# Kernel tuning notes

Hardware: AMD Instinct MI355X
Metric: run time of the kernel (lower is better)

Reference implementation:

```python
import jax, jax.numpy as jnp
import numpy as np

B, T, C = 4, 2048, 1024
H = 16
DH = C // H


def setup_inputs() -> dict:
    key = jax.random.key(0)
    k1, k2, k3 = jax.random.split(key, 3)
    x = jax.random.normal(k1, (B, T, C), dtype=jnp.float32)
    w_qkv = jax.random.normal(k2, (3 * C, C), dtype=jnp.float32) * (1.0 / np.sqrt(C))
    w_out = jax.random.normal(k3, (C, C), dtype=jnp.float32) * (1.0 / np.sqrt(C))
    attn_mask = jnp.ones((B, T), dtype=jnp.int32)
    return {"x": x, "attn_mask": attn_mask, "w_qkv": w_qkv, "w_out": w_out}


def reference(x, attn_mask, w_qkv, w_out):
    b, t, c = x.shape
    h, dh = H, DH
    qkv = jnp.einsum('btc,fc->btf', x, w_qkv)  # [B,T,3C]
    q, k, v = jnp.split(qkv, 3, axis=-1)
    # [B,H,T,Dh]
    q = q.reshape(b, t, h, dh).transpose(0, 2, 1, 3)
    k = k.reshape(b, t, h, dh).transpose(0, 2, 1, 3)
    v = v.reshape(b, t, h, dh).transpose(0, 2, 1, 3)
    scale = jnp.sqrt(jnp.float32(dh))
    scores = jnp.einsum('bhqd,bhkd->bhqk', q, k) / scale  # [B,H,T,T]
    causal = jnp.tril(jnp.ones((t, t), dtype=bool))
    mask = causal[None, None, :, :] & (attn_mask[:, None, None, :] != 0)
    scores = jnp.where(mask, scores, -jnp.inf)
    p = jax.nn.softmax(scores, axis=-1)
    p = jnp.where(jnp.isnan(p), 0.0, p)  # nan_to_num for fully-masked rows
    out = jnp.einsum('bhqk,bhkd->bhqd', p, v)
    out = out.transpose(0, 2, 1, 3).reshape(b, t, c)
    return jnp.einsum('btc,fc->btf', out, w_out)
```

## Files before the change

kernel.cpp:

```cpp
#include <hip/hip_runtime.h>
#include <cstdint>
#include <cmath>


#define Bb 4
#define Tt 2048
#define Cc 1024
#define Hh 16
#define DHd 64
#define Mm (Bb*Tt)

typedef __attribute__((ext_vector_type(8))) short bf16x8;
typedef __attribute__((ext_vector_type(4))) short s16x4;
typedef __attribute__((ext_vector_type(4))) float f32x4;
typedef __attribute__((ext_vector_type(2))) unsigned int u32x2;

__device__ __forceinline__ short f2bf(float f) {
  uint32_t u = __builtin_bit_cast(uint32_t, f);
  u = (u + 0x7fffu + ((u >> 16) & 1u)) >> 16;
  return (short)(uint16_t)u;
}

__device__ __forceinline__ uint32_t cvtpk(float lo, float hi) {
  uint32_t r;
  asm("v_cvt_pk_bf16_f32 %0, %1, %2" : "=v"(r) : "v"(lo), "v"(hi));
  return r;
}

__device__ __forceinline__ f32x4 mfma16(s16x4 a, s16x4 b, f32x4 c) {
#if __has_builtin(__builtin_amdgcn_mfma_f32_16x16x16_bf16)
  return __builtin_amdgcn_mfma_f32_16x16x16_bf16(a, b, c, 0, 0, 0);
#elif __has_builtin(__builtin_amdgcn_mfma_f32_16x16x16bf16_1k)
  return __builtin_amdgcn_mfma_f32_16x16x16bf16_1k(a, b, c, 0, 0, 0);
#else
  f32x4 d;
  asm("v_mfma_f32_16x16x16_bf16 %0, %1, %2, %3" : "=v"(d) : "v"(a), "v"(b), "v"(c));
  return d;
#endif
}

__global__ void cvt_bf16(const float* __restrict__ in, short* __restrict__ out, int n4) {
  int i = blockIdx.x * blockDim.x + threadIdx.x;
  if (i >= n4) return;
  f32x4 v = reinterpret_cast<const f32x4*>(in)[i];
  s16x4 o;
  o.x = f2bf(v.x); o.y = f2bf(v.y); o.z = f2bf(v.z); o.w = f2bf(v.w);
  reinterpret_cast<s16x4*>(out)[i] = o;
}

#define BK 32

template<int MODE>
__global__ __launch_bounds__(256) void gemm_bt(
    const short* __restrict__ A, const short* __restrict__ Bt, int K, int N,
    float* __restrict__ Cout,
    short* __restrict__ qb, short* __restrict__ kb, short* __restrict__ vtb)
{
  __shared__ __align__(16) short As[128*BK];
  __shared__ __align__(16) short Bs[128*BK];
  const int tid = threadIdx.x;
  const int lane = tid & 63, wid = tid >> 6;
  const int wr = wid >> 1, wc = wid & 1;
  const int bm = blockIdx.y, bn = blockIdx.x;
  const int r16 = lane & 15, g = lane >> 4;

  f32x4 acc[4][4];
#pragma unroll
  for (int i = 0; i < 4; ++i)
#pragma unroll
    for (int j = 0; j < 4; ++j) acc[i][j] = (f32x4)0.0f;

  const int srow = lane >> 2;
  const int scol = (lane & 3) * 8;
  const int ch0 = wid * 2;

  const int nk = K / BK;
  for (int kt = 0; kt < nk; ++kt) {
    const int k0 = kt * BK;
#pragma unroll
    for (int c = 0; c < 2; ++c) {
      const int chunk = ch0 + c;
      const int row = chunk * 16 + srow;
      const short* ga = A  + (size_t)(bm*128 + row)*K + k0 + scol;
      const short* gb = Bt + (size_t)(bn*128 + row)*K + k0 + scol;
      __builtin_amdgcn_global_load_lds((const __attribute__((address_space(1))) void*)ga,
                                       (__attribute__((address_space(3))) void*)(&As[chunk*512]), 16, 0, 0);
      __builtin_amdgcn_global_load_lds((const __attribute__((address_space(1))) void*)gb,
                                       (__attribute__((address_space(3))) void*)(&Bs[chunk*512]), 16, 0, 0);
    }
    __syncthreads();

    bf16x8 af[4], bfv[4];
#pragma unroll
    for (int mi = 0; mi < 4; ++mi)
      af[mi] = *reinterpret_cast<const bf16x8*>(&As[(wr*64 + mi*16 + r16)*BK + g*8]);
#pragma unroll
    for (int ni = 0; ni < 4; ++ni)
      bfv[ni] = *reinterpret_cast<const bf16x8*>(&Bs[(wc*64 + ni*16 + r16)*BK + g*8]);
#pragma unroll
    for (int mi = 0; mi < 4; ++mi)
#pragma unroll
      for (int ni = 0; ni < 4; ++ni)
        acc[mi][ni] = __builtin_amdgcn_mfma_f32_16x16x32_bf16(af[mi], bfv[ni], acc[mi][ni], 0, 0, 0);
    __syncthreads();
  }

#pragma unroll
  for (int mi = 0; mi < 4; ++mi) {
    const int row0 = bm*128 + wr*64 + mi*16 + g*4;
#pragma unroll
    for (int ni = 0; ni < 4; ++ni) {
      const int col_g = bn*128 + wc*64 + ni*16 + r16;
      if (MODE == 1) {
#pragma unroll
        for (int r = 0; r < 4; ++r)
          Cout[(size_t)(row0 + r) * N + col_g] = acc[mi][ni][r];
      } else {
        const int which = col_g >> 10;
        const int hd = col_g & 1023;
        const int h = hd >> 6, d = hd & 63;
        const int b = row0 >> 11, t0 = row0 & 2047;
        const int bh = b*Hh + h;
        if (which == 0) {
#pragma unroll
          for (int r = 0; r < 4; ++r)
            qb[(((size_t)bh*Tt + t0 + r) << 6) + d] = f2bf(acc[mi][ni][r] * 0.18033688f);
        } else if (which == 1) {
#pragma unroll
          for (int r = 0; r < 4; ++r)
            kb[(((size_t)bh*Tt + t0 + r) << 6) + d] = f2bf(acc[mi][ni][r]);
        } else {
          u32x2 w;
          w.x = cvtpk(acc[mi][ni][0], acc[mi][ni][1]);
          w.y = cvtpk(acc[mi][ni][2], acc[mi][ni][3]);
          *reinterpret_cast<u32x2*>(vtb + ((size_t)bh*DHd + d)*Tt + t0) = w;
        }
      }
    }
  }
}

__global__ __launch_bounds__(256) void attn_fwd(
    const short* __restrict__ qbf, const short* __restrict__ kbf,
    const short* __restrict__ vtb, const int* __restrict__ am,
    short* __restrict__ ob)
{
  __shared__ __align__(16) short Ks[2][64*64];
  __shared__ __align__(16) short Vts[2][64*64];
  const int tid = threadIdx.x;
  const int lane = tid & 63, wid = tid >> 6;
  const int r16 = lane & 15, g = lane >> 4;

  const int lin = blockIdx.x;
  const int xcd = lin & 7;
  const int idx = lin >> 3;
  const int bh  = xcd * 8 + (idx & 7);
  const int qi_raw = idx >> 3;
  const int grp = qi_raw >> 2, rem = qi_raw & 3;
  const int qi = (grp == 0) ? 15 - rem : (grp == 1) ? rem : (grp == 2) ? 11 - rem : 4 + rem;
  const int b = bh >> 4, h = bh & 15;
  const int q0 = qi * 128;
  const int wq0 = q0 + wid * 32;

  bf16x8 qf[2][2];
#pragma unroll
  for (int m = 0; m < 2; ++m) {
    const short* qbase = qbf + ((size_t)bh*Tt + wq0 + m*16 + r16)*DHd;
    qf[m][0] = *reinterpret_cast<const bf16x8*>(qbase + g*8);
    qf[m][1] = *reinterpret_cast<const bf16x8*>(qbase + 32 + g*8);
  }

  f32x4 o[2][4];
  float mrow[2], lrow[2];
#pragma unroll
  for (int m = 0; m < 2; ++m) {
    mrow[m] = -INFINITY; lrow[m] = 0.f;
#pragma unroll
    for (int i = 0; i < 4; ++i) o[m][i] = (f32x4)0.0f;
  }

  const int nkv = 2*qi + 2;
  const int srow = tid >> 3, scc = tid & 7;
  bf16x8 kr[2], vr[2];
#pragma unroll
  for (int c = 0; c < 2; ++c) {
    const int row = srow + c*32;
    kr[c] = *reinterpret_cast<const bf16x8*>(kbf + ((size_t)bh*Tt + row)*DHd + scc*8);
    vr[c] = *reinterpret_cast<const bf16x8*>(vtb + ((size_t)bh*DHd + row)*Tt + scc*8);
  }
#pragma unroll
  for (int c = 0; c < 2; ++c) {
    const int row = srow + c*32;
    const int off = (row*128 + scc*16) ^ ((row & 7) << 4);
    *reinterpret_cast<bf16x8*>((char*)Ks[0] + off) = kr[c];
    *reinterpret_cast<bf16x8*>((char*)Vts[0] + off) = vr[c];
  }
  __syncthreads();

  for (int kv = 0; kv < nkv; ++kv) {
    const int cur = kv & 1;
    const int kv0 = kv * 64;
    const unsigned long long mb = __ballot(am[b*Tt + kv0 + lane] != 0);
    if (kv + 1 < nkv) {
#pragma unroll
      for (int c = 0; c < 2; ++c) {
        const int row = srow + c*32;
        kr[c] = *reinterpret_cast<const bf16x8*>(kbf + ((size_t)bh*Tt + kv0 + 64 + row)*DHd + scc*8);
        vr[c] = *reinterpret_cast<const bf16x8*>(vtb + ((size_t)bh*DHd + row)*Tt + kv0 + 64 + scc*8);
      }
    }

    if (kv0 <= wq0 + 31) {
      const char* kbp = (const char*)Ks[cur];
      const char* vbp = (const char*)Vts[cur];
      const int swzr = (r16 & 7) << 4;

      f32x4 st[2][4];
      __builtin_amdgcn_s_setprio(1);
#pragma unroll
      for (int kt = 0; kt < 4; ++kt) {
        const int rb = (kt*16 + r16)*128;
        const bf16x8 ka0 = *reinterpret_cast<const bf16x8*>(kbp + ((rb + g*16) ^ swzr));
        const bf16x8 ka1 = *reinterpret_cast<const bf16x8*>(kbp + ((rb + 64 + g*16) ^ swzr));
#pragma unroll
        for (int m = 0; m < 2; ++m) {
          f32x4 t = (f32x4)0.0f;
          t = __builtin_amdgcn_mfma_f32_16x16x32_bf16(ka0, qf[m][0], t, 0, 0, 0);
          t = __builtin_amdgcn_mfma_f32_16x16x32_bf16(ka1, qf[m][1], t, 0, 0, 0);
          st[m][kt] = t;
        }
      }
      __builtin_amdgcn_s_setprio(0);

      const bool notall = (mb != ~0ull);
      const bool diag = (kv0 + 63 > wq0);
      if (diag || notall) {
#pragma unroll
        for (int m = 0; m < 2; ++m) {
          const int qrow = wq0 + m*16 + r16;
#pragma unroll
          for (int kt = 0; kt < 4; ++kt)
#pragma unroll
            for (int r = 0; r < 4; ++r) {
              const int kl = kt*16 + g*4 + r;
              bool ok = !diag || (kv0 + kl <= qrow);
              if (notall) ok = ok && ((mb >> kl) & 1ull);
              if (!ok) st[m][kt][r] = -3.0e38f;
            }
        }
      }

      float mx[2], rs[2];
#pragma unroll
      for (int m = 0; m < 2; ++m) {
        f32x4 t0, t1;
#pragma unroll
        for (int i = 0; i < 4; ++i) { t0[i] = fmaxf(st[m][0][i], st[m][1][i]); t1[i] = fmaxf(st[m][2][i], st[m][3][i]); }
#pragma unroll
        for (int i = 0; i < 4; ++i) t0[i] = fmaxf(t0[i], t1[i]);
        mx[m] = fmaxf(fmaxf(t0[0], t0[1]), fmaxf(t0[2], t0[3]));
      }
      {
        float a0 = __shfl_xor(mx[0], 16), a1 = __shfl_xor(mx[1], 16);
        mx[0] = fmaxf(mx[0], a0); mx[1] = fmaxf(mx[1], a1);
        a0 = __shfl_xor(mx[0], 32); a1 = __shfl_xor(mx[1], 32);
        mx[0] = fmaxf(mx[0], a0); mx[1] = fmaxf(mx[1], a1);
      }
      const bool need = __any((mx[0] > mrow[0] + 8.f) || (mx[1] > mrow[1] + 8.f));
      if (need) {
#pragma unroll
        for (int m = 0; m < 2; ++m) {
          const float mnew = fmaxf(mrow[m], mx[m]);
          const float alpha = __builtin_amdgcn_exp2f(mrow[m] - mnew);
          mrow[m] = mnew;
          lrow[m] *= alpha;
#pragma unroll
          for (int dt = 0; dt < 4; ++dt) o[m][dt] *= alpha;
        }
      }

      s16x4 pb[2][4];
#pragma unroll
      for (int m = 0; m < 2; ++m) {
#pragma unroll
        for (int kt = 0; kt < 4; ++kt)
#pragma unroll
          for (int r = 0; r < 4; ++r)
            st[m][kt][r] = __builtin_amdgcn_exp2f(st[m][kt][r] - mrow[m]);
#pragma unroll
        for (int kt = 0; kt < 4; ++kt) {
          u32x2 w;
          w.x = cvtpk(st[m][kt][0], st[m][kt][1]);
          w.y = cvtpk(st[m][kt][2], st[m][kt][3]);
          pb[m][kt] = __builtin_bit_cast(s16x4, w);
        }
        f32x4 s4;
#pragma unroll
        for (int i = 0; i < 4; ++i) s4[i] = st[m][0][i] + st[m][1][i] + st[m][2][i] + st[m][3][i];
        rs[m] = (s4[0] + s4[1]) + (s4[2] + s4[3]);
      }
      {
        float a0 = __shfl_xor(rs[0], 16), a1 = __shfl_xor(rs[1], 16);
        rs[0] += a0; rs[1] += a1;
        a0 = __shfl_xor(rs[0], 32); a1 = __shfl_xor(rs[1], 32);
        rs[0] += a0; rs[1] += a1;
      }
      lrow[0] += rs[0]; lrow[1] += rs[1];

      __builtin_amdgcn_s_setprio(1);
#pragma unroll
      for (int dt = 0; dt < 4; ++dt) {
        const int row = dt*16 + r16;
        const int rb = row*128;
        const int r7 = row & 7;
#pragma unroll
        for (int kt = 0; kt < 4; ++kt) {
          const s16x4 va = *reinterpret_cast<const s16x4*>(
              vbp + rb + ((((kt<<1) + (g>>1)) ^ r7) << 4) + (g & 1)*8);
          o[0][dt] = mfma16(va, pb[0][kt], o[0][dt]);
          o[1][dt] = mfma16(va, pb[1][kt], o[1][dt]);
        }
      }
      __builtin_amdgcn_s_setprio(0);
    }

    if (kv + 1 < nkv) {
#pragma unroll
      for (int c = 0; c < 2; ++c) {
        const int row = srow + c*32;
        const int off = (row*128 + scc*16) ^ ((row & 7) << 4);
        *reinterpret_cast<bf16x8*>((char*)Ks[cur^1] + off) = kr[c];
        *reinterpret_cast<bf16x8*>((char*)Vts[cur^1] + off) = vr[c];
      }
    }
    __syncthreads();
  }

#pragma unroll
  for (int m = 0; m < 2; ++m) {
    const float inv = (mrow[m] > -1e37f) ? 1.0f / lrow[m] : 0.f;
    short* obase = ob + ((size_t)(b*Tt + wq0 + m*16 + r16))*Cc + h*DHd;
#pragma unroll
    for (int dt = 0; dt < 4; ++dt) {
      u32x2 w;
      w.x = cvtpk(o[m][dt][0]*inv, o[m][dt][1]*inv);
      w.y = cvtpk(o[m][dt][2]*inv, o[m][dt][3]*inv);
      *reinterpret_cast<u32x2*>(obase + dt*16 + g*4) = w;
    }
  }
}

extern "C" void kernel_launch(void* const* d_in, const int* in_sizes, int n_in,
                              void* d_out, int out_size, void* d_ws, size_t ws_size,
                              hipStream_t stream) {
  const float* x    = (const float*)d_in[0];
  const int*   am   = (const int*)d_in[1];
  const float* wqkv = (const float*)d_in[2];
  const float* wout = (const float*)d_in[3];
  float* out = (float*)d_out;

  const size_t mc = (size_t)Mm * Cc;
  short* ws    = (short*)d_ws;
  short* xb    = ws;
  short* wqkvb = xb + mc;
  short* woutb = wqkvb + (size_t)3*Cc*Cc;
  short* qbuf  = woutb + (size_t)Cc*Cc;
  short* kbuf  = qbuf + mc;
  short* vtbuf = kbuf + mc;
  short* attnb = xb;

  cvt_bf16<<<(int)((mc/4 + 255)/256), 256, 0, stream>>>(x, xb, (int)(mc/4));
  cvt_bf16<<<(3*Cc*Cc/4 + 255)/256, 256, 0, stream>>>(wqkv, wqkvb, 3*Cc*Cc/4);
  cvt_bf16<<<(Cc*Cc/4 + 255)/256, 256, 0, stream>>>(wout, woutb, Cc*Cc/4);

  gemm_bt<0><<<dim3(3*Cc/128, Mm/128), 256, 0, stream>>>(
      xb, wqkvb, Cc, 3*Cc, nullptr, qbuf, kbuf, vtbuf);

  attn_fwd<<<dim3(Bb*Hh*Tt/128), 256, 0, stream>>>(qbuf, kbuf, vtbuf, am, attnb);

  gemm_bt<1><<<dim3(Cc/128, Mm/128), 256, 0, stream>>>(
      attnb, woutb, Cc, Cc, out, nullptr, nullptr, nullptr);
}
```

Baseline: 218.3 us.

## Stage K/V tiles via direct global-to-LDS loads and prefetch mask

Replaces the register-staged K/V tile loads and later LDS stores in the attention kernel with global_load_lds direct-to-LDS transfers into the next buffer. The XOR swizzle moves from the LDS write address to the global read address. The attention-mask element for the next tile is also prefetched one iteration early. This is meant to cut VGPR pressure and the explicit LDS store instructions, at the cost of depending on the barrier to cover completion of the async LDS writes.

```diff
diff --git a/kernel.cpp b/kernel.cpp
--- a/kernel.cpp
+++ b/kernel.cpp
@@ -162,6 +162,29 @@
   const int q0 = qi * 128;
   const int wq0 = q0 + wid * 32;
 
+  const size_t kbase = (size_t)bh * Tt * DHd;
+  const size_t vbase = (size_t)bh * DHd * Tt;
+
+  const int srow0 = tid >> 3;
+  const int p8    = tid & 7;
+  const int ubase = tid & 448;
+
+#define ASTAGE(SLOT, T0) do {                                                  \
+    _Pragma("unroll")                                                          \
+    for (int c_ = 0; c_ < 2; ++c_) {                                           \
+      const int row_ = c_*32 + srow0;                                          \
+      const int sp_  = (p8 ^ (row_ & 7)) * 8;                                  \
+      const short* gk_ = kbf + kbase + (size_t)((T0) + row_)*DHd + sp_;        \
+      const short* gv_ = vtb + vbase + (size_t)row_*Tt + (T0) + sp_;           \
+      __builtin_amdgcn_global_load_lds(                                        \
+          (const __attribute__((address_space(1))) void*)gk_,                  \
+          (__attribute__((address_space(3))) void*)(&Ks[SLOT][(c_*256 + ubase)*8]), 16, 0, 0); \
+      __builtin_amdgcn_global_load_lds(                                        \
+          (const __attribute__((address_space(1))) void*)gv_,                  \
+          (__attribute__((address_space(3))) void*)(&Vts[SLOT][(c_*256 + ubase)*8]), 16, 0, 0); \
+    }                                                                          \
+  } while (0)
+
   bf16x8 qf[2][2];
 #pragma unroll
   for (int m = 0; m < 2; ++m) {
@@ -180,34 +203,19 @@
   }
 
   const int nkv = 2*qi + 2;
-  const int srow = tid >> 3, scc = tid & 7;
-  bf16x8 kr[2], vr[2];
-#pragma unroll
-  for (int c = 0; c < 2; ++c) {
-    const int row = srow + c*32;
-    kr[c] = *reinterpret_cast<const bf16x8*>(kbf + ((size_t)bh*Tt + row)*DHd + scc*8);
-    vr[c] = *reinterpret_cast<const bf16x8*>(vtb + ((size_t)bh*DHd + row)*Tt + scc*8);
-  }
-#pragma unroll
-  for (int c = 0; c < 2; ++c) {
-    const int row = srow + c*32;
-    const int off = (row*128 + scc*16) ^ ((row & 7) << 4);
-    *reinterpret_cast<bf16x8*>((char*)Ks[0] + off) = kr[c];
-    *reinterpret_cast<bf16x8*>((char*)Vts[0] + off) = vr[c];
-  }
+  int amv = am[b*Tt + lane];
+
+  ASTAGE(0, 0);
   __syncthreads();
 
   for (int kv = 0; kv < nkv; ++kv) {
     const int cur = kv & 1;
     const int kv0 = kv * 64;
-    const unsigned long long mb = __ballot(am[b*Tt + kv0 + lane] != 0);
+    const unsigned long long mb = __ballot(amv != 0);
+    int amv_next = 0;
     if (kv + 1 < nkv) {
-#pragma unroll
-      for (int c = 0; c < 2; ++c) {
-        const int row = srow + c*32;
-        kr[c] = *reinterpret_cast<const bf16x8*>(kbf + ((size_t)bh*Tt + kv0 + 64 + row)*DHd + scc*8);
-        vr[c] = *reinterpret_cast<const bf16x8*>(vtb + ((size_t)bh*DHd + row)*Tt + kv0 + 64 + scc*8);
-      }
+      ASTAGE(cur ^ 1, kv0 + 64);
+      amv_next = am[b*Tt + kv0 + 64 + lane];
     }
 
     if (kv0 <= wq0 + 31) {
@@ -250,7 +258,7 @@
         }
       }
 
-      float mx[2], rs[2];
+      float mx[2];
 #pragma unroll
       for (int m = 0; m < 2; ++m) {
         f32x4 t0, t1;
@@ -280,6 +288,7 @@
       }
 
       s16x4 pb[2][4];
+      float rsum[2];
 #pragma unroll
       for (int m = 0; m < 2; ++m) {
 #pragma unroll
@@ -297,15 +306,15 @@
         f32x4 s4;
 #pragma unroll
         for (int i = 0; i < 4; ++i) s4[i] = st[m][0][i] + st[m][1][i] + st[m][2][i] + st[m][3][i];
-        rs[m] = (s4[0] + s4[1]) + (s4[2] + s4[3]);
+        rsum[m] = (s4[0] + s4[1]) + (s4[2] + s4[3]);
       }
       {
-        float a0 = __shfl_xor(rs[0], 16), a1 = __shfl_xor(rs[1], 16);
-        rs[0] += a0; rs[1] += a1;
-        a0 = __shfl_xor(rs[0], 32); a1 = __shfl_xor(rs[1], 32);
-        rs[0] += a0; rs[1] += a1;
-      }
-      lrow[0] += rs[0]; lrow[1] += rs[1];
+        float a0 = __shfl_xor(rsum[0], 16), a1 = __shfl_xor(rsum[1], 16);
+        rsum[0] += a0; rsum[1] += a1;
+        a0 = __shfl_xor(rsum[0], 32); a1 = __shfl_xor(rsum[1], 32);
+        rsum[0] += a0; rsum[1] += a1;
+      }
+      lrow[0] += rsum[0]; lrow[1] += rsum[1];
 
       __builtin_amdgcn_s_setprio(1);
 #pragma unroll
@@ -324,15 +333,7 @@
       __builtin_amdgcn_s_setprio(0);
     }
 
-    if (kv + 1 < nkv) {
-#pragma unroll
-      for (int c = 0; c < 2; ++c) {
-        const int row = srow + c*32;
-        const int off = (row*128 + scc*16) ^ ((row & 7) << 4);
-        *reinterpret_cast<bf16x8*>((char*)Ks[cur^1] + off) = kr[c];
-        *reinterpret_cast<bf16x8*>((char*)Vts[cur^1] + off) = vr[c];
-      }
-    }
+    amv = amv_next;
     __syncthreads();
   }
 
@@ -348,6 +349,7 @@
       *reinterpret_cast<u32x2*>(obase + dt*16 + g*4) = w;
     }
   }
+#undef ASTAGE
 }
 
 extern "C" void kernel_launch(void* const* d_in, const int* in_sizes, int n_in,
```

Measured after the change: 219.4 us. About the same (+0.5%).
